# Optimization experiments

Measured on AMD Instinct MI355X. Metric: run time of the kernel, lower is better.

## Reference

```python
import jax, jax.numpy as jnp
import numpy as np

EPS = 1e-5


def setup_inputs() -> dict:
    key = jax.random.key(0)
    ks = jax.random.split(key, 4)
    b, c, h, w = 4, 256, 64, 64
    x = jax.random.normal(ks[0], (b, c, h, w), dtype=jnp.float32)
    W_qkv = jax.random.normal(ks[1], (3 * c, c), dtype=jnp.float32) * (1.0 / np.sqrt(c))
    b_qkv = jnp.zeros((3 * c,), dtype=jnp.float32)
    W_out = jax.random.normal(ks[2], (c, c), dtype=jnp.float32) * (1.0 / np.sqrt(c))
    b_out = jnp.zeros((c,), dtype=jnp.float32)
    gamma = jnp.ones((c,), dtype=jnp.float32)
    beta = jnp.zeros((c,), dtype=jnp.float32)
    return {"x": x, "W_qkv": W_qkv, "b_qkv": b_qkv, "W_out": W_out,
            "b_out": b_out, "gamma": gamma, "beta": beta}


def reference(x, W_qkv, b_qkv, W_out, b_out, gamma, beta):
    b, c, h, w = x.shape
    n = h * w  # number of spatial tokens

    # BatchNorm2d (training mode: batch statistics over b,h,w per channel)
    mean = jnp.mean(x, axis=(0, 2, 3), keepdims=True)
    var = jnp.var(x, axis=(0, 2, 3), keepdims=True)
    x_norm = (x - mean) * jax.lax.rsqrt(var + EPS)
    x_norm = x_norm * gamma[None, :, None, None] + beta[None, :, None, None]

    # 1x1 conv to QKV: [b, 3c, h, w]
    qkv = jnp.einsum('bchw,oc->bohw', x_norm, W_qkv) + b_qkv[None, :, None, None]
    q, k, v = jnp.split(qkv, 3, axis=1)

    q = q.transpose(0, 2, 3, 1).reshape(b, n, c)  # [b, n, c]
    k = k.reshape(b, c, n)                         # [b, c, n]
    v = v.transpose(0, 2, 3, 1).reshape(b, n, c)  # [b, n, c]

    scale = c ** (-0.5)
    dot = jnp.einsum('bqc,bck->bqk', q, k) * scale  # [b, n, n]
    attn = jax.nn.softmax(dot, axis=-1)
    out = jnp.einsum('bqk,bkc->bqc', attn, v)       # [b, n, c]
    out = out.reshape(b, h, w, c).transpose(0, 3, 1, 2)  # [b, c, h, w]

    # 1x1 output conv + residual
    out = jnp.einsum('bchw,oc->bohw', out, W_out) + b_out[None, :, None, None]
    return out + x
```

## Files before the change

### kernel.cpp

```cpp
#include <hip/hip_runtime.h>
#include <hip/hip_bf16.h>

typedef __attribute__((ext_vector_type(4))) float f32x4;
typedef __attribute__((ext_vector_type(8))) short bf16x8;
typedef __attribute__((ext_vector_type(4))) unsigned int u32x4;

#define BB 4
#define C 256
#define N 4096
#define TS 32
#define EPSI 1e-5f

constexpr size_t BBNC = (size_t)BB * N * C;

__device__ __forceinline__ unsigned short f2bf(float f) {
    unsigned int u = __builtin_bit_cast(unsigned int, f);
    u += 0x7fffu + ((u >> 16) & 1u);
    return (unsigned short)(u >> 16);
}

__device__ __forceinline__ float bf2f(unsigned short h) {
    unsigned int u = ((unsigned int)h) << 16;
    return __builtin_bit_cast(float, u);
}

__device__ __forceinline__ unsigned int cvt_pk_bf16(float lo, float hi) {
    unsigned int r;
    asm("v_cvt_pk_bf16_f32 %0, %1, %2" : "=v"(r) : "v"(lo), "v"(hi));
    return r;
}

__device__ __forceinline__ void stage16(const unsigned short* g, unsigned short* l) {
    __builtin_amdgcn_global_load_lds(
        (const __attribute__((address_space(1))) void*)g,
        (__attribute__((address_space(3))) void*)l, 16, 0, 0);
}

__global__ __launch_bounds__(256) void bn_stats_k(
    const float* __restrict__ x, const float* __restrict__ gamma,
    const float* __restrict__ beta, float* __restrict__ scale, float* __restrict__ shift,
    const float* __restrict__ Wqkv, unsigned short* __restrict__ wqkv_bf,
    const float* __restrict__ Wout, unsigned short* __restrict__ wout_bf)
{
    int tid = threadIdx.x;
    if (blockIdx.x >= C) {
        int cb = blockIdx.x - C;
        const float* src;
        unsigned short* dst;
        size_t i;
        if (cb < 96) { src = Wqkv; dst = wqkv_bf; i = (size_t)cb * 256 + tid; }
        else         { src = Wout; dst = wout_bf; i = (size_t)(cb - 96) * 256 + tid; }
        const float4* p = (const float4*)(src + i * 8);
        float4 a = p[0], c = p[1];
        unsigned int pk[4];
        pk[0] = cvt_pk_bf16(a.x, a.y);
        pk[1] = cvt_pk_bf16(a.z, a.w);
        pk[2] = cvt_pk_bf16(c.x, c.y);
        pk[3] = cvt_pk_bf16(c.z, c.w);
        *(u32x4*)(dst + i * 8) = *(u32x4*)pk;
        return;
    }
    int c = blockIdx.x;
    float s = 0.f, s2 = 0.f;
    for (int b = 0; b < BB; ++b) {
        const float4* p = (const float4*)(x + ((size_t)b * C + c) * N);
        for (int i = tid; i < N / 4; i += 256) {
            float4 v = p[i];
            s  += v.x + v.y + v.z + v.w;
            s2 += v.x * v.x + v.y * v.y + v.z * v.z + v.w * v.w;
        }
    }
    for (int m = 1; m < 64; m <<= 1) {
        s  += __shfl_xor(s, m);
        s2 += __shfl_xor(s2, m);
    }
    __shared__ float rs[4], rs2[4];
    int w = tid >> 6;
    if ((tid & 63) == 0) { rs[w] = s; rs2[w] = s2; }
    __syncthreads();
    if (tid == 0) {
        float S  = rs[0] + rs[1] + rs[2] + rs[3];
        float S2 = rs2[0] + rs2[1] + rs2[2] + rs2[3];
        const float inv_n = 1.f / (BB * N);
        float mean = S * inv_n;
        float var  = S2 * inv_n - mean * mean;
        float sc = gamma[c] * rsqrtf(var + EPSI);
        scale[c] = sc;
        shift[c] = beta[c] - mean * sc;
    }
}

__global__ __launch_bounds__(256) void qkv_gemm_k(
    const float* __restrict__ x, const unsigned short* __restrict__ wqkv_bf,
    const float* __restrict__ bqkv,
    const float* __restrict__ scale, const float* __restrict__ shift,
    unsigned short* __restrict__ q, unsigned short* __restrict__ kt, unsigned short* __restrict__ v)
{
    __shared__ unsigned short Alds[32 * 264];
    __shared__ unsigned short Wlds[64 * 256];

    int tid = threadIdx.x;
    int b  = blockIdx.y;
    int T0 = blockIdx.x * 32;
    int lane = tid & 63;
    int w = tid >> 6;
    int wm = w >> 1, wn = w & 1;
    int g = lane >> 4, l15 = lane & 15;

    {
        int cbase = tid >> 1;
        int t0 = (tid & 1) * 16;
#pragma unroll
        for (int pass = 0; pass < 2; ++pass) {
            int cc = cbase + pass * 128;
            const float4* xp = (const float4*)(x + ((size_t)b * C + cc) * N + T0 + t0);
            float sc = scale[cc], sh = shift[cc];
#pragma unroll
            for (int j = 0; j < 4; ++j) {
                float4 vv = xp[j];
                int t = t0 + j * 4;
                Alds[(t + 0) * 264 + cc] = f2bf(vv.x * sc + sh);
                Alds[(t + 1) * 264 + cc] = f2bf(vv.y * sc + sh);
                Alds[(t + 2) * 264 + cc] = f2bf(vv.z * sc + sh);
                Alds[(t + 3) * 264 + cc] = f2bf(vv.w * sc + sh);
            }
        }
    }

    const float QSCALE = 0.0625f * 1.44269504088896f;

    for (int oi = 0; oi < 12; ++oi) {
        int O0 = oi * 64;
        __syncthreads();
        {
            const unsigned short* wb = wqkv_bf + (size_t)O0 * 256;
#pragma unroll
            for (int j = 0; j < 8; ++j) {
                int qq = tid + j * 256;
                int lo = qq >> 5, sc2 = qq & 31;
                stage16(wb + (size_t)lo * 256 + ((sc2 ^ (lo & 7)) * 8), &Wlds[qq * 8]);
            }
        }
        __syncthreads();

        f32x4 acc[2];
        acc[0] = f32x4{0.f, 0.f, 0.f, 0.f};
        acc[1] = f32x4{0.f, 0.f, 0.f, 0.f};
#pragma unroll
        for (int kk = 0; kk < 8; ++kk) {
            bf16x8 afr = *(const bf16x8*)&Alds[(wm * 16 + l15) * 264 + kk * 32 + g * 8];
#pragma unroll
            for (int nf = 0; nf < 2; ++nf) {
                int lo = wn * 32 + nf * 16 + l15;
                bf16x8 bfr = *(const bf16x8*)&Wlds[lo * 256 + (((kk * 4 + g) ^ (lo & 7)) * 8)];
                acc[nf] = __builtin_amdgcn_mfma_f32_16x16x32_bf16(afr, bfr, acc[nf], 0, 0, 0);
            }
        }

#pragma unroll
        for (int nf = 0; nf < 2; ++nf) {
            int o = O0 + wn * 32 + nf * 16 + l15;
            float bias = bqkv[o];
#pragma unroll
            for (int r = 0; r < 4; ++r) {
                int t = T0 + wm * 16 + g * 4 + r;
                float val = acc[nf][r] + bias;
                if (O0 < 256) {
                    q[((size_t)b * N + t) * C + o] = f2bf(val * QSCALE);
                } else if (O0 < 512) {
                    kt[((size_t)b * N + t) * C + (o - 256)] = f2bf(val);
                } else {
                    int tp = (t & ~31) | ((g * 2 + wm) * 4 + r);
                    v[((size_t)b * C + (o - 512)) * N + tp] = f2bf(val);
                }
            }
        }
    }
}

template<int NSEG>
__global__ __launch_bounds__(256, 2) void attn_k(
    const unsigned short* __restrict__ q, const unsigned short* __restrict__ kt,
    const unsigned short* __restrict__ v,
    unsigned short* __restrict__ P, float* __restrict__ ml)
{
    constexpr int NS  = N / NSEG;
    constexpr int NIT = NS / TS;
    __shared__ unsigned short Klds[2][TS * 256];
    __shared__ unsigned short Vlds[2][256 * TS];

    int tid = threadIdx.x;
    int h  = blockIdx.y;
    int b  = blockIdx.z;
    int Q0 = blockIdx.x * 128;
    int lane = tid & 63;
    int lw = tid >> 6;
    int g = lane >> 4, l15 = lane & 15;

    bf16x8 qf[2][8];
#pragma unroll
    for (int m = 0; m < 2; ++m) {
        const unsigned short* qp = q + ((size_t)b * N + Q0 + lw * 32 + m * 16 + l15) * C + g * 8;
#pragma unroll
        for (int kc = 0; kc < 8; ++kc)
            qf[m][kc] = *(const bf16x8*)(qp + kc * 32);
    }

    f32x4 oacc[2][16];
#pragma unroll
    for (int m = 0; m < 2; ++m)
#pragma unroll
        for (int i = 0; i < 16; ++i) oacc[m][i] = f32x4{0.f, 0.f, 0.f, 0.f};
    float mrow[2] = {-1e30f, -1e30f};
    float lg[2]   = {0.f, 0.f};

    const unsigned short* kb = kt + ((size_t)b * N + h * NS) * C;
    const unsigned short* vb = v + (size_t)b * C * N + h * NS;

#define STAGE_K(buf_, t_)                                                            \
    {                                                                                \
        const unsigned short* kbt = kb + (size_t)(t_) * TS * 256;                    \
        _Pragma("unroll")                                                            \
        for (int j = 0; j < 4; ++j) {                                                \
            int qq = tid + j * 256;                                                  \
            int tk = qq >> 5, sc = qq & 31;                                          \
            stage16(kbt + tk * 256 + ((sc ^ (tk & 7)) * 8), &Klds[buf_][qq * 8]);    \
        }                                                                            \
    }
#define STAGE_V(buf_, t_)                                                            \
    {                                                                                \
        _Pragma("unroll")                                                            \
        for (int j = 0; j < 4; ++j) {                                                \
            int qq = tid + j * 256;                                                  \
            int c = qq >> 2, sl = qq & 3;                                            \
            stage16(vb + (size_t)c * N + (t_) * TS + ((sl ^ ((c >> 1) & 3)) * 8),    \
                    &Vlds[buf_][qq * 8]);                                            \
        }                                                                            \
    }

    STAGE_K(0, 0);
    STAGE_V(0, 0);
    __syncthreads();

    bf16x8 pf[2];

    for (int t = 0; t < NIT; ++t) {
        int s = t & 1;
        if (t + 1 < NIT) STAGE_K(s ^ 1, t + 1);

        f32x4 st[2][2];
#pragma unroll
        for (int m = 0; m < 2; ++m)
#pragma unroll
            for (int ct = 0; ct < 2; ++ct) st[m][ct] = f32x4{0.f, 0.f, 0.f, 0.f};
        __builtin_amdgcn_s_setprio(1);
#pragma unroll
        for (int kc = 0; kc < 8; ++kc) {
#pragma unroll
            for (int ct = 0; ct < 2; ++ct) {
                int tk = ct * 16 + l15;
                int slot = (kc * 4 + g) ^ (tk & 7);
                bf16x8 kf = *(const bf16x8*)&Klds[s][tk * 256 + slot * 8];
                st[0][ct] = __builtin_amdgcn_mfma_f32_16x16x32_bf16(kf, qf[0][kc], st[0][ct], 0, 0, 0);
                st[1][ct] = __builtin_amdgcn_mfma_f32_16x16x32_bf16(kf, qf[1][kc], st[1][ct], 0, 0, 0);
            }
        }
        __builtin_amdgcn_s_setprio(0);

        if (t > 0) {
            __builtin_amdgcn_s_setprio(1);
#pragma unroll
            for (int cf = 0; cf < 16; ++cf) {
                int c = cf * 16 + l15;
                int vslot = g ^ ((c >> 1) & 3);
                bf16x8 vf = *(const bf16x8*)&Vlds[s ^ 1][c * TS + vslot * 8];
                oacc[0][cf] = __builtin_amdgcn_mfma_f32_16x16x32_bf16(vf, pf[0], oacc[0][cf], 0, 0, 0);
                oacc[1][cf] = __builtin_amdgcn_mfma_f32_16x16x32_bf16(vf, pf[1], oacc[1][cf], 0, 0, 0);
            }
            __builtin_amdgcn_s_setprio(0);
        }

        float mx[2];
#pragma unroll
        for (int m = 0; m < 2; ++m)
            mx[m] = fmaxf(fmaxf(fmaxf(st[m][0][0], st[m][0][1]), fmaxf(st[m][0][2], st[m][0][3])),
                          fmaxf(fmaxf(st[m][1][0], st[m][1][1]), fmaxf(st[m][1][2], st[m][1][3])));
        bool ok = (mx[0] - mrow[0] <= 8.f) & (mx[1] - mrow[1] <= 8.f);
        if (!__all(ok)) {
#pragma unroll
            for (int m = 0; m < 2; ++m) {
                float v0 = mx[m];
                v0 = fmaxf(v0, __shfl_xor(v0, 16));
                v0 = fmaxf(v0, __shfl_xor(v0, 32));
                float mn = fmaxf(mrow[m], v0);
                float alpha = exp2f(mrow[m] - mn);
                mrow[m] = mn;
                lg[m] *= alpha;
#pragma unroll
                for (int f = 0; f < 16; ++f)
#pragma unroll
                    for (int r = 0; r < 4; ++r) oacc[m][f][r] *= alpha;
            }
        }
#pragma unroll
        for (int m = 0; m < 2; ++m) {
            float rs = 0.f;
#pragma unroll
            for (int ct = 0; ct < 2; ++ct)
#pragma unroll
                for (int r = 0; r < 4; ++r) {
                    float p = exp2f(st[m][ct][r] - mrow[m]);
                    st[m][ct][r] = p;
                    rs += p;
                }
            lg[m] += rs;
            u32x4 pk;
            pk[0] = cvt_pk_bf16(st[m][0][0], st[m][0][1]);
            pk[1] = cvt_pk_bf16(st[m][0][2], st[m][0][3]);
            pk[2] = cvt_pk_bf16(st[m][1][0], st[m][1][1]);
            pk[3] = cvt_pk_bf16(st[m][1][2], st[m][1][3]);
            pf[m] = __builtin_bit_cast(bf16x8, pk);
        }

        __syncthreads();
        if (t + 1 < NIT) STAGE_V(s ^ 1, t + 1);
    }

    {
        int s = (NIT - 1) & 1;
#pragma unroll
        for (int cf = 0; cf < 16; ++cf) {
            int c = cf * 16 + l15;
            int vslot = g ^ ((c >> 1) & 3);
            bf16x8 vf = *(const bf16x8*)&Vlds[s][c * TS + vslot * 8];
            oacc[0][cf] = __builtin_amdgcn_mfma_f32_16x16x32_bf16(vf, pf[0], oacc[0][cf], 0, 0, 0);
            oacc[1][cf] = __builtin_amdgcn_mfma_f32_16x16x32_bf16(vf, pf[1], oacc[1][cf], 0, 0, 0);
        }
    }

    float lt[2];
#pragma unroll
    for (int m = 0; m < 2; ++m) {
        float v0 = lg[m];
        v0 += __shfl_xor(v0, 16);
        v0 += __shfl_xor(v0, 32);
        lt[m] = v0;
    }
#pragma unroll
    for (int m = 0; m < 2; ++m) {
        size_t tokid = (size_t)b * N + Q0 + lw * 32 + m * 16 + l15;
        if (g == 0) {
            ml[(size_t)(2 * h + 0) * (BB * N) + tokid] = mrow[m];
            ml[(size_t)(2 * h + 1) * (BB * N) + tokid] = lt[m];
        }
        unsigned short* pp = P + (size_t)h * BBNC + tokid * C;
#pragma unroll
        for (int cf = 0; cf < 16; ++cf) {
#pragma unroll
            for (int rp = 0; rp < 2; ++rp) {
                int c = cf * 16 + g * 4 + rp * 2;
                unsigned int pk2 = cvt_pk_bf16(oacc[m][cf][rp * 2 + 0], oacc[m][cf][rp * 2 + 1]);
                *(unsigned int*)&pp[c] = pk2;
            }
        }
    }
}

template<int NSEG>
__global__ __launch_bounds__(256) void out_gemm_k(
    const unsigned short* __restrict__ P, const float* __restrict__ ml,
    const unsigned short* __restrict__ wout_bf, const float* __restrict__ bout,
    const float* __restrict__ x, float* __restrict__ out)
{
    __shared__ unsigned short Alds[256 * 40];
    __shared__ unsigned short Blds[32 * 40];

    int tid = threadIdx.x;
    int b  = blockIdx.y;
    int T0 = blockIdx.x * 32;
    int lane = tid & 63;
    int w = tid >> 6;
    int g = lane >> 4, l15 = lane & 15;

    int tl = (tid >> 2) & 31;
    float cw[NSEG], cinv;
    {
        size_t tok = (size_t)b * N + T0 + tl;
        float ms[NSEG], ls[NSEG];
#pragma unroll
        for (int s = 0; s < NSEG; ++s) {
            ms[s] = ml[(size_t)(2 * s + 0) * (BB * N) + tok];
            ls[s] = ml[(size_t)(2 * s + 1) * (BB * N) + tok];
        }
        float M = ms[0];
#pragma unroll
        for (int s = 1; s < NSEG; ++s) M = fmaxf(M, ms[s]);
        float den = 0.f;
#pragma unroll
        for (int s = 0; s < NSEG; ++s) {
            cw[s] = exp2f(ms[s] - M);
            den += cw[s] * ls[s];
        }
        cinv = 1.f / den;
    }

    f32x4 acc[4][2];
#pragma unroll
    for (int i = 0; i < 4; ++i)
#pragma unroll
        for (int j = 0; j < 2; ++j) acc[i][j] = f32x4{0.f, 0.f, 0.f, 0.f};

    for (int c0 = 0; c0 < C; c0 += 32) {
        if (c0) __syncthreads();
        {
            const unsigned short* wp = wout_bf + (size_t)tid * C + c0;
#pragma unroll
            for (int jj = 0; jj < 4; ++jj)
                *(bf16x8*)&Alds[tid * 40 + jj * 8] = *(const bf16x8*)(wp + jj * 8);
        }
        if (tid < 128) {
            int j = tid & 3;
            size_t base = ((size_t)b * N + T0 + tl) * C + c0 + j * 8;
            float val[8];
#pragma unroll
            for (int e = 0; e < 8; ++e) val[e] = 0.f;
#pragma unroll
            for (int s = 0; s < NSEG; ++s) {
                bf16x8 p = *(const bf16x8*)(P + (size_t)s * BBNC + base);
                float wgt = cw[s];
#pragma unroll
                for (int e = 0; e < 8; ++e) val[e] += wgt * bf2f((unsigned short)p[e]);
            }
            unsigned int opk[4];
#pragma unroll
            for (int jj = 0; jj < 4; ++jj)
                opk[jj] = cvt_pk_bf16(val[2 * jj] * cinv, val[2 * jj + 1] * cinv);
            *(u32x4*)&Blds[tl * 40 + j * 8] = *(u32x4*)opk;
        }
        __syncthreads();

        bf16x8 afr[4];
#pragma unroll
        for (int mf = 0; mf < 4; ++mf)
            afr[mf] = *(const bf16x8*)&Alds[(w * 64 + mf * 16 + l15) * 40 + g * 8];
#pragma unroll
        for (int tf = 0; tf < 2; ++tf) {
            bf16x8 bfr = *(const bf16x8*)&Blds[(tf * 16 + l15) * 40 + g * 8];
#pragma unroll
            for (int mf = 0; mf < 4; ++mf)
                acc[mf][tf] = __builtin_amdgcn_mfma_f32_16x16x32_bf16(afr[mf], bfr, acc[mf][tf], 0, 0, 0);
        }
    }

#pragma unroll
    for (int mf = 0; mf < 4; ++mf) {
#pragma unroll
        for (int tf = 0; tf < 2; ++tf) {
            int t = T0 + tf * 16 + l15;
#pragma unroll
            for (int r = 0; r < 4; ++r) {
                int co = w * 64 + mf * 16 + g * 4 + r;
                size_t oidx = ((size_t)b * C + co) * N + t;
                out[oidx] = acc[mf][tf][r] + bout[co] + x[oidx];
            }
        }
    }
}

extern "C" void kernel_launch(void* const* d_in, const int* in_sizes, int n_in,
                              void* d_out, int out_size, void* d_ws, size_t ws_size,
                              hipStream_t stream) {
    const float* x     = (const float*)d_in[0];
    const float* Wqkv  = (const float*)d_in[1];
    const float* bqkv  = (const float*)d_in[2];
    const float* Wout  = (const float*)d_in[3];
    const float* bout  = (const float*)d_in[4];
    const float* gamma = (const float*)d_in[5];
    const float* beta  = (const float*)d_in[6];
    float* out = (float*)d_out;

    char* ws = (char*)d_ws;
    float* scale = (float*)ws;
    float* shift = (float*)(ws + 1024);
    unsigned short* wout_bf = (unsigned short*)(ws + 4096);
    unsigned short* q  = wout_bf + (size_t)C * C;
    unsigned short* kt = q  + BBNC;
    unsigned short* v  = kt + BBNC;
    unsigned short* P  = v  + BBNC;
    unsigned short* wqkv_bf = P;

    size_t need4 = 4096 + (size_t)C * C * 2 + 7 * BBNC * 2 + (size_t)8 * BB * N * 4;

    bn_stats_k<<<dim3(C + 128), dim3(256), 0, stream>>>(x, gamma, beta, scale, shift,
                                                        Wqkv, wqkv_bf, Wout, wout_bf);
    qkv_gemm_k<<<dim3(N / 32, BB), dim3(256), 0, stream>>>(x, wqkv_bf, bqkv, scale, shift, q, kt, v);

    if (ws_size >= need4) {
        float* ml = (float*)(P + 4 * BBNC);
        attn_k<4><<<dim3(N / 128, 4, BB), dim3(256), 0, stream>>>(q, kt, v, P, ml);
        out_gemm_k<4><<<dim3(N / 32, BB), dim3(256), 0, stream>>>(P, ml, wout_bf, bout, x, out);
    } else {
        float* ml = (float*)(P + 2 * BBNC);
        attn_k<2><<<dim3(N / 128, 2, BB), dim3(256), 0, stream>>>(q, kt, v, P, ml);
        out_gemm_k<2><<<dim3(N / 32, BB), dim3(256), 0, stream>>>(P, ml, wout_bf, bout, x, out);
    }
}
```

Before: 152.3 us.

## Replace software-pipelined PV matmul with in-iteration K/V staging and compute

Removes the one-step software pipeline in which the P·V MFMAs for tile t-1 were interleaved with the QK^T of tile t and V was staged after a barrier. Now K and V for the next tile are staged together at the top of the loop, and P·V for the current tile runs right after softmax in the same iteration, followed by one barrier. This simplifies the schedule and shortens the live range of the P fragments, but it loses the overlap of softmax latency with the previous tile's PV MFMAs.

New measurement: 141.4 us, median of 2. 7.2% less time.

```diff
diff --git a/kernel.cpp b/kernel.cpp
--- a/kernel.cpp
+++ b/kernel.cpp
@@ -217,7 +217,7 @@
     const unsigned short* kb = kt + ((size_t)b * N + h * NS) * C;
     const unsigned short* vb = v + (size_t)b * C * N + h * NS;
 
-#define STAGE_K(buf_, t_)                                                            \
+#define STAGE(buf_, t_)                                                              \
     {                                                                                \
         const unsigned short* kbt = kb + (size_t)(t_) * TS * 256;                    \
         _Pragma("unroll")                                                            \
@@ -226,9 +226,6 @@
             int tk = qq >> 5, sc = qq & 31;                                          \
             stage16(kbt + tk * 256 + ((sc ^ (tk & 7)) * 8), &Klds[buf_][qq * 8]);    \
         }                                                                            \
-    }
-#define STAGE_V(buf_, t_)                                                            \
-    {                                                                                \
         _Pragma("unroll")                                                            \
         for (int j = 0; j < 4; ++j) {                                                \
             int qq = tid + j * 256;                                                  \
@@ -238,15 +235,12 @@
         }                                                                            \
     }
 
-    STAGE_K(0, 0);
-    STAGE_V(0, 0);
+    STAGE(0, 0);
     __syncthreads();
 
-    bf16x8 pf[2];
-
     for (int t = 0; t < NIT; ++t) {
-        int s = t & 1;
-        if (t + 1 < NIT) STAGE_K(s ^ 1, t + 1);
+        int cur = t & 1;
+        if (t < NIT - 1) STAGE(cur ^ 1, t + 1);
 
         f32x4 st[2][2];
 #pragma unroll
@@ -260,25 +254,12 @@
             for (int ct = 0; ct < 2; ++ct) {
                 int tk = ct * 16 + l15;
                 int slot = (kc * 4 + g) ^ (tk & 7);
-                bf16x8 kf = *(const bf16x8*)&Klds[s][tk * 256 + slot * 8];
+                bf16x8 kf = *(const bf16x8*)&Klds[cur][tk * 256 + slot * 8];
                 st[0][ct] = __builtin_amdgcn_mfma_f32_16x16x32_bf16(kf, qf[0][kc], st[0][ct], 0, 0, 0);
                 st[1][ct] = __builtin_amdgcn_mfma_f32_16x16x32_bf16(kf, qf[1][kc], st[1][ct], 0, 0, 0);
             }
         }
         __builtin_amdgcn_s_setprio(0);
-
-        if (t > 0) {
-            __builtin_amdgcn_s_setprio(1);
-#pragma unroll
-            for (int cf = 0; cf < 16; ++cf) {
-                int c = cf * 16 + l15;
-                int vslot = g ^ ((c >> 1) & 3);
-                bf16x8 vf = *(const bf16x8*)&Vlds[s ^ 1][c * TS + vslot * 8];
-                oacc[0][cf] = __builtin_amdgcn_mfma_f32_16x16x32_bf16(vf, pf[0], oacc[0][cf], 0, 0, 0);
-                oacc[1][cf] = __builtin_amdgcn_mfma_f32_16x16x32_bf16(vf, pf[1], oacc[1][cf], 0, 0, 0);
-            }
-            __builtin_amdgcn_s_setprio(0);
-        }
 
         float mx[2];
 #pragma unroll
@@ -302,6 +283,7 @@
                     for (int r = 0; r < 4; ++r) oacc[m][f][r] *= alpha;
             }
         }
+        bf16x8 pf[2];
 #pragma unroll
         for (int m = 0; m < 2; ++m) {
             float rs = 0.f;
@@ -322,20 +304,17 @@
             pf[m] = __builtin_bit_cast(bf16x8, pk);
         }
 
-        __syncthreads();
-        if (t + 1 < NIT) STAGE_V(s ^ 1, t + 1);
-    }
-
-    {
-        int s = (NIT - 1) & 1;
+        __builtin_amdgcn_s_setprio(1);
 #pragma unroll
         for (int cf = 0; cf < 16; ++cf) {
             int c = cf * 16 + l15;
             int vslot = g ^ ((c >> 1) & 3);
-            bf16x8 vf = *(const bf16x8*)&Vlds[s][c * TS + vslot * 8];
+            bf16x8 vf = *(const bf16x8*)&Vlds[cur][c * TS + vslot * 8];
             oacc[0][cf] = __builtin_amdgcn_mfma_f32_16x16x32_bf16(vf, pf[0], oacc[0][cf], 0, 0, 0);
             oacc[1][cf] = __builtin_amdgcn_mfma_f32_16x16x32_bf16(vf, pf[1], oacc[1][cf], 0, 0, 0);
         }
+        __builtin_amdgcn_s_setprio(0);
+        __syncthreads();
     }
 
     float lt[2];
```
